# Kernel optimization log

Hardware: AMD Instinct MI355X
Metric: run time of the kernel (lower is better)

## Reference

```python
import jax, jax.numpy as jnp
import numpy as np

B, T, D = 64, 2048, 512
UNITS = 10  # hardcoded in original module


def setup_inputs() -> dict:
    key = jax.random.key(0)
    ks = jax.random.split(key, 6)
    Eo = jax.random.normal(ks[0], (B, T, D), dtype=jnp.float32)
    H = jax.random.normal(ks[1], (B, D), dtype=jnp.float32)
    # Keras Dense params: kernel [in, out], bias [out] (glorot-ish scale)
    W_eo = jax.random.normal(ks[2], (D, UNITS), dtype=jnp.float32) * (1.0 / np.sqrt(D))
    b_eo = jnp.zeros((UNITS,), dtype=jnp.float32)
    W_h = jax.random.normal(ks[3], (D, UNITS), dtype=jnp.float32) * (1.0 / np.sqrt(D))
    b_h = jnp.zeros((UNITS,), dtype=jnp.float32)
    W_s = jax.random.normal(ks[4], (UNITS, 1), dtype=jnp.float32) * (1.0 / np.sqrt(UNITS))
    b_s = jnp.zeros((1,), dtype=jnp.float32)
    return {"Eo": Eo, "H": H, "W_eo": W_eo, "b_eo": b_eo,
            "W_h": W_h, "b_h": b_h, "W_s": W_s, "b_s": b_s}


def reference(Eo, H, W_eo, b_eo, W_h, b_h, W_s, b_s):
    # Eo: [B, T, D], H: [B, D]
    Eo_d = jnp.einsum('btd,du->btu', Eo, W_eo) + b_eo          # [B, T, U]
    H_d = H @ W_h + b_h                                        # [B, U]
    EoH = jnp.tanh(Eo_d + H_d[:, None, :])                     # [B, T, U]
    score = jnp.einsum('btu,uo->bto', EoH, W_s) + b_s          # [B, T, 1]
    weight = jax.nn.softmax(score, axis=1)                     # softmax over T
    context = jnp.sum(Eo * weight, axis=1)                     # [B, D]
    return (context, weight)
```

## Files before the change

kernel.cpp:

```cpp
#include <hip/hip_runtime.h>
#include <math.h>

#define BB 64
#define TT 2048
#define DD 512
#define UU 10
#define S_CHUNKS 16
#define CHUNK_T (TT / S_CHUNKS)
#define NB (CHUNK_T / 16)

__device__ __forceinline__ float fast_tanh(float x) {
    return 1.0f - 2.0f / (1.0f + __expf(2.0f * x));
}

template<int K>
__device__ __forceinline__ float dpp_shr(float x) {
    int xi = __builtin_bit_cast(int, x);
    int r  = __builtin_amdgcn_update_dpp(0, xi, 0x110 | K, 0xF, 0xF, true);
    return __builtin_bit_cast(float, r);
}

__device__ __forceinline__ float read_lane_f(float v, int lane) {
    return __builtin_bit_cast(float,
        __builtin_amdgcn_readlane(__builtin_bit_cast(int, v), lane));
}

__global__ __launch_bounds__(256) void attn_pass1(
    const float* __restrict__ Eo, const float* __restrict__ H,
    const float* __restrict__ W_eo, const float* __restrict__ b_eo,
    const float* __restrict__ W_h, const float* __restrict__ b_h,
    const float* __restrict__ W_s, const float* __restrict__ b_s,
    float* __restrict__ pexp, float* __restrict__ pc)
{
    const int b     = blockIdx.y;
    const int chunk = blockIdx.x;
    const int tid   = threadIdx.x;
    const int wave  = tid >> 6;
    const int lane  = tid & 63;

    float hacc[UU];
    #pragma unroll
    for (int u = 0; u < UU; ++u) hacc[u] = 0.f;
    const float* Hb = H + (size_t)b * DD;
    #pragma unroll
    for (int k = 0; k < DD / 64; ++k) {
        float hv = Hb[k * 64 + lane];
        const float* wr = W_h + (size_t)(k * 64 + lane) * UU;
        #pragma unroll
        for (int u = 0; u < UU; ++u) hacc[u] += hv * wr[u];
    }
    #pragma unroll
    for (int off = 1; off < 64; off <<= 1) {
        #pragma unroll
        for (int u = 0; u < UU; ++u) hacc[u] += __shfl_xor(hacc[u], off, 64);
    }
    float hb[UU];
    #pragma unroll
    for (int u = 0; u < UU; ++u) hb[u] = hacc[u] + b_h[u] + b_eo[u];

    float wsv[UU];
    #pragma unroll
    for (int u = 0; u < UU; ++u) wsv[u] = W_s[u];
    const float bs = b_s[0];

    float wv[8][UU];
    #pragma unroll
    for (int k = 0; k < 2; ++k) {
        #pragma unroll
        for (int j = 0; j < 4; ++j) {
            const float* wr = W_eo + (size_t)(k * 256 + 4 * lane + j) * UU;
            #pragma unroll
            for (int u = 0; u < UU; ++u) wv[k * 4 + j][u] = wr[u];
        }
    }

    float l = 0.f;
    float c[8];
    #pragma unroll
    for (int j = 0; j < 8; ++j) c[j] = 0.f;

    const int  t0w  = chunk * CHUNK_T + wave * (CHUNK_T / 4);
    const bool lo32 = (lane & 32) == 0;
    const bool lo16 = (lane & 16) == 0;
    const float* rowbase = Eo + (size_t)b * TT * DD + 4 * lane;

    for (int i = 0; i < NB; ++i) {
        const int tb = t0w + i * 4;

        float e[4][8];
        #pragma unroll
        for (int tt = 0; tt < 4; ++tt) {
            const float* row = rowbase + (size_t)(tb + tt) * DD;
            float4 e0 = *(const float4*)(row);
            float4 e1 = *(const float4*)(row + 256);
            e[tt][0] = e0.x; e[tt][1] = e0.y; e[tt][2] = e0.z; e[tt][3] = e0.w;
            e[tt][4] = e1.x; e[tt][5] = e1.y; e[tt][6] = e1.z; e[tt][7] = e1.w;
        }

        float acc[4][UU];
        #pragma unroll
        for (int tt = 0; tt < 4; ++tt) {
            #pragma unroll
            for (int u = 0; u < UU; ++u) acc[tt][u] = 0.f;
            #pragma unroll
            for (int j = 0; j < 8; ++j) {
                #pragma unroll
                for (int u = 0; u < UU; ++u) acc[tt][u] += e[tt][j] * wv[j][u];
            }
        }

        float s = bs;
        #pragma unroll
        for (int u = 0; u < UU; ++u) {
            float y0 = lo32 ? acc[0][u] : acc[2][u];
            float o0 = lo32 ? acc[2][u] : acc[0][u];
            y0 += __shfl_xor(o0, 32, 64);
            float y1 = lo32 ? acc[1][u] : acc[3][u];
            float o1 = lo32 ? acc[3][u] : acc[1][u];
            y1 += __shfl_xor(o1, 32, 64);
            float z  = lo16 ? y0 : y1;
            float oz = lo16 ? y1 : y0;
            z += __shfl_xor(oz, 16, 64);
            z += dpp_shr<1>(z);
            z += dpp_shr<2>(z);
            z += dpp_shr<4>(z);
            z += dpp_shr<8>(z);
            s += wsv[u] * fast_tanh(z + hb[u]);
        }
        float p = __expf(s);

        if ((lane & 15) == 15) pexp[(size_t)b * TT + tb + (lane >> 4)] = p;

        float p0 = read_lane_f(p, 15);
        float p1 = read_lane_f(p, 31);
        float p2 = read_lane_f(p, 47);
        float p3 = read_lane_f(p, 63);
        l += (p0 + p1) + (p2 + p3);
        #pragma unroll
        for (int j = 0; j < 8; ++j)
            c[j] += p0 * e[0][j] + p1 * e[1][j] + p2 * e[2][j] + p3 * e[3][j];
    }

    __shared__ float sc[4][DD];
    #pragma unroll
    for (int k = 0; k < 2; ++k) {
        #pragma unroll
        for (int j = 0; j < 4; ++j)
            sc[wave][k * 256 + 4 * lane + j] = c[k * 4 + j];
    }
    __syncthreads();

    const int pidx = b * S_CHUNKS + chunk;
    for (int d = tid; d < DD; d += 256) {
        pc[(size_t)pidx * DD + d] = (sc[0][d] + sc[1][d]) + (sc[2][d] + sc[3][d]);
    }
}

__global__ __launch_bounds__(256) void attn_epilogue(
    const float* __restrict__ pexp, const float* __restrict__ pc,
    float* __restrict__ ctx_out, float* __restrict__ wout)
{
    const int b = blockIdx.x;
    const int tid = threadIdx.x;
    const int wave = tid >> 6;

    float s = 0.f;
    #pragma unroll
    for (int k = 0; k < TT / 256; ++k) s += pexp[(size_t)b * TT + k * 256 + tid];
    #pragma unroll
    for (int off = 1; off < 64; off <<= 1) s += __shfl_xor(s, off, 64);

    __shared__ float sl[4];
    if ((tid & 63) == 0) sl[wave] = s;
    __syncthreads();
    const float l = (sl[0] + sl[1]) + (sl[2] + sl[3]);
    const float inv = 1.0f / l;

    for (int d = tid; d < DD; d += 256) {
        float v = 0.f;
        #pragma unroll
        for (int sss = 0; sss < S_CHUNKS; ++sss)
            v += pc[((size_t)(b * S_CHUNKS + sss)) * DD + d];
        ctx_out[(size_t)b * DD + d] = v * inv;
    }
    for (int t = tid; t < TT; t += 256)
        wout[(size_t)b * TT + t] = pexp[(size_t)b * TT + t] * inv;
}

extern "C" void kernel_launch(void* const* d_in, const int* in_sizes, int n_in,
                              void* d_out, int out_size, void* d_ws, size_t ws_size,
                              hipStream_t stream) {
    const float* Eo   = (const float*)d_in[0];
    const float* H    = (const float*)d_in[1];
    const float* W_eo = (const float*)d_in[2];
    const float* b_eo = (const float*)d_in[3];
    const float* W_h  = (const float*)d_in[4];
    const float* b_h  = (const float*)d_in[5];
    const float* W_s  = (const float*)d_in[6];
    const float* b_s  = (const float*)d_in[7];

    float* pexp = (float*)d_ws;
    float* pc   = pexp + (size_t)BB * TT;

    float* out_ctx = (float*)d_out;
    float* out_w   = out_ctx + (size_t)BB * DD;

    dim3 gridA(S_CHUNKS, BB);
    attn_pass1<<<gridA, 256, 0, stream>>>(Eo, H, W_eo, b_eo, W_h, b_h, W_s, b_s,
                                          pexp, pc);
    attn_epilogue<<<BB, 256, 0, stream>>>(pexp, pc, out_ctx, out_w);
}
```

Measured before the change: 65.56 us.

## Process two timesteps per wave iteration and split epilogue across four blocks per batch

New measurement: 74.42 us. +13.5%, slower.

```diff
diff --git a/kernel.cpp b/kernel.cpp
--- a/kernel.cpp
+++ b/kernel.cpp
@@ -7,7 +7,7 @@
 #define UU 10
 #define S_CHUNKS 16
 #define CHUNK_T (TT / S_CHUNKS)
-#define NB (CHUNK_T / 16)
+#define NB (CHUNK_T / 8)
 
 __device__ __forceinline__ float fast_tanh(float x) {
     return 1.0f - 2.0f / (1.0f + __expf(2.0f * x));
@@ -81,15 +81,14 @@
 
     const int  t0w  = chunk * CHUNK_T + wave * (CHUNK_T / 4);
     const bool lo32 = (lane & 32) == 0;
-    const bool lo16 = (lane & 16) == 0;
     const float* rowbase = Eo + (size_t)b * TT * DD + 4 * lane;
 
     for (int i = 0; i < NB; ++i) {
-        const int tb = t0w + i * 4;
-
-        float e[4][8];
-        #pragma unroll
-        for (int tt = 0; tt < 4; ++tt) {
+        const int tb = t0w + i * 2;
+
+        float e[2][8];
+        #pragma unroll
+        for (int tt = 0; tt < 2; ++tt) {
             const float* row = rowbase + (size_t)(tb + tt) * DD;
             float4 e0 = *(const float4*)(row);
             float4 e1 = *(const float4*)(row + 256);
@@ -97,9 +96,9 @@
             e[tt][4] = e1.x; e[tt][5] = e1.y; e[tt][6] = e1.z; e[tt][7] = e1.w;
         }
 
-        float acc[4][UU];
-        #pragma unroll
-        for (int tt = 0; tt < 4; ++tt) {
+        float acc[2][UU];
+        #pragma unroll
+        for (int tt = 0; tt < 2; ++tt) {
             #pragma unroll
             for (int u = 0; u < UU; ++u) acc[tt][u] = 0.f;
             #pragma unroll
@@ -112,33 +111,27 @@
         float s = bs;
         #pragma unroll
         for (int u = 0; u < UU; ++u) {
-            float y0 = lo32 ? acc[0][u] : acc[2][u];
-            float o0 = lo32 ? acc[2][u] : acc[0][u];
-            y0 += __shfl_xor(o0, 32, 64);
-            float y1 = lo32 ? acc[1][u] : acc[3][u];
-            float o1 = lo32 ? acc[3][u] : acc[1][u];
-            y1 += __shfl_xor(o1, 32, 64);
-            float z  = lo16 ? y0 : y1;
-            float oz = lo16 ? y1 : y0;
-            z += __shfl_xor(oz, 16, 64);
-            z += dpp_shr<1>(z);
-            z += dpp_shr<2>(z);
-            z += dpp_shr<4>(z);
-            z += dpp_shr<8>(z);
-            s += wsv[u] * fast_tanh(z + hb[u]);
+            float y = lo32 ? acc[0][u] : acc[1][u];
+            float o = lo32 ? acc[1][u] : acc[0][u];
+            y += __shfl_xor(o, 32, 64);
+            y += __shfl_xor(y, 16, 64);
+            y += dpp_shr<1>(y);
+            y += dpp_shr<2>(y);
+            y += dpp_shr<4>(y);
+            y += dpp_shr<8>(y);
+            s += wsv[u] * fast_tanh(y + hb[u]);
         }
         float p = __expf(s);
 
-        if ((lane & 15) == 15) pexp[(size_t)b * TT + tb + (lane >> 4)] = p;
+        if (lane == 15) pexp[(size_t)b * TT + tb]     = p;
+        if (lane == 47) pexp[(size_t)b * TT + tb + 1] = p;
 
         float p0 = read_lane_f(p, 15);
-        float p1 = read_lane_f(p, 31);
-        float p2 = read_lane_f(p, 47);
-        float p3 = read_lane_f(p, 63);
-        l += (p0 + p1) + (p2 + p3);
+        float p1 = read_lane_f(p, 47);
+        l += p0 + p1;
         #pragma unroll
         for (int j = 0; j < 8; ++j)
-            c[j] += p0 * e[0][j] + p1 * e[1][j] + p2 * e[2][j] + p3 * e[3][j];
+            c[j] += p0 * e[0][j] + p1 * e[1][j];
     }
 
     __shared__ float sc[4][DD];
@@ -160,8 +153,9 @@
     const float* __restrict__ pexp, const float* __restrict__ pc,
     float* __restrict__ ctx_out, float* __restrict__ wout)
 {
-    const int b = blockIdx.x;
-    const int tid = threadIdx.x;
+    const int b    = blockIdx.x >> 2;
+    const int part = blockIdx.x & 3;
+    const int tid  = threadIdx.x;
     const int wave = tid >> 6;
 
     float s = 0.f;
@@ -176,15 +170,19 @@
     const float l = (sl[0] + sl[1]) + (sl[2] + sl[3]);
     const float inv = 1.0f / l;
 
-    for (int d = tid; d < DD; d += 256) {
+    const int d = part * (DD / 4) + tid;
+    if (tid < DD / 4) {
         float v = 0.f;
         #pragma unroll
         for (int sss = 0; sss < S_CHUNKS; ++sss)
             v += pc[((size_t)(b * S_CHUNKS + sss)) * DD + d];
         ctx_out[(size_t)b * DD + d] = v * inv;
     }
-    for (int t = tid; t < TT; t += 256)
+    #pragma unroll
+    for (int k = 0; k < 2; ++k) {
+        const int t = part * (TT / 4) + k * 256 + tid;
         wout[(size_t)b * TT + t] = pexp[(size_t)b * TT + t] * inv;
+    }
 }
 
 extern "C" void kernel_launch(void* const* d_in, const int* in_sizes, int n_in,
@@ -208,5 +206,5 @@
     dim3 gridA(S_CHUNKS, BB);
     attn_pass1<<<gridA, 256, 0, stream>>>(Eo, H, W_eo, b_eo, W_h, b_h, W_s, b_s,
                                           pexp, pc);
-    attn_epilogue<<<BB, 256, 0, stream>>>(pexp, pc, out_ctx, out_w);
-}
+    attn_epilogue<<<BB * 4, 256, 0, stream>>>(pexp, pc, out_ctx, out_w);
+}
```

## Double-buffer Eo rows via global_load_lds DMA and split epilogue across blocks

Applied to the files above, without the earlier changes.

Measured after the change: 65.32 us. About the same (-0.4%).

```diff
diff --git a/kernel.cpp b/kernel.cpp
--- a/kernel.cpp
+++ b/kernel.cpp
@@ -23,6 +23,12 @@
 __device__ __forceinline__ float read_lane_f(float v, int lane) {
     return __builtin_bit_cast(float,
         __builtin_amdgcn_readlane(__builtin_bit_cast(int, v), lane));
+}
+
+typedef __attribute__((address_space(1))) const void gvoid;
+typedef __attribute__((address_space(3))) void lvoid;
+__device__ __forceinline__ void dma16(const float* g, float* l) {
+    __builtin_amdgcn_global_load_lds((gvoid*)g, (lvoid*)l, 16, 0, 0);
 }
 
 __global__ __launch_bounds__(256) void attn_pass1(
@@ -38,6 +44,9 @@
     const int wave  = tid >> 6;
     const int lane  = tid & 63;
 
+    __shared__ __align__(16) float buf[4][2][4][DD];
+    __shared__ float sc[4][DD];
+
     float hacc[UU];
     #pragma unroll
     for (int u = 0; u < UU; ++u) hacc[u] = 0.f;
@@ -82,17 +91,33 @@
     const int  t0w  = chunk * CHUNK_T + wave * (CHUNK_T / 4);
     const bool lo32 = (lane & 32) == 0;
     const bool lo16 = (lane & 16) == 0;
-    const float* rowbase = Eo + (size_t)b * TT * DD + 4 * lane;
-
-    for (int i = 0; i < NB; ++i) {
+    const float* rowb = Eo + (size_t)b * TT * DD + 4 * lane;
+
+    #pragma unroll
+    for (int tt = 0; tt < 4; ++tt) {
+        const float* g = rowb + (size_t)(t0w + tt) * DD;
+        dma16(g,       &buf[wave][0][tt][0]);
+        dma16(g + 256, &buf[wave][0][tt][256]);
+    }
+
+    auto do_batch = [&](int i) {
+        const int cur = i & 1, nxt = cur ^ 1;
+        if (i + 1 < NB) {
+            #pragma unroll
+            for (int tt = 0; tt < 4; ++tt) {
+                const float* g = rowb + (size_t)(t0w + (i + 1) * 4 + tt) * DD;
+                dma16(g,       &buf[wave][nxt][tt][0]);
+                dma16(g + 256, &buf[wave][nxt][tt][256]);
+            }
+        }
+        __builtin_amdgcn_sched_barrier(0);
+
         const int tb = t0w + i * 4;
-
         float e[4][8];
         #pragma unroll
         for (int tt = 0; tt < 4; ++tt) {
-            const float* row = rowbase + (size_t)(tb + tt) * DD;
-            float4 e0 = *(const float4*)(row);
-            float4 e1 = *(const float4*)(row + 256);
+            float4 e0 = *(const float4*)&buf[wave][cur][tt][4 * lane];
+            float4 e1 = *(const float4*)&buf[wave][cur][tt][256 + 4 * lane];
             e[tt][0] = e0.x; e[tt][1] = e0.y; e[tt][2] = e0.z; e[tt][3] = e0.w;
             e[tt][4] = e1.x; e[tt][5] = e1.y; e[tt][6] = e1.z; e[tt][7] = e1.w;
         }
@@ -139,9 +164,17 @@
         #pragma unroll
         for (int j = 0; j < 8; ++j)
             c[j] += p0 * e[0][j] + p1 * e[1][j] + p2 * e[2][j] + p3 * e[3][j];
-    }
-
-    __shared__ float sc[4][DD];
+    };
+
+    asm volatile("s_waitcnt vmcnt(0)" ::: "memory");
+    __builtin_amdgcn_sched_barrier(0);
+    do_batch(0);
+    for (int i = 1; i < NB; ++i) {
+        asm volatile("s_waitcnt vmcnt(1)" ::: "memory");
+        __builtin_amdgcn_sched_barrier(0);
+        do_batch(i);
+    }
+
     #pragma unroll
     for (int k = 0; k < 2; ++k) {
         #pragma unroll
@@ -160,8 +193,9 @@
     const float* __restrict__ pexp, const float* __restrict__ pc,
     float* __restrict__ ctx_out, float* __restrict__ wout)
 {
-    const int b = blockIdx.x;
-    const int tid = threadIdx.x;
+    const int b    = blockIdx.x >> 2;
+    const int part = blockIdx.x & 3;
+    const int tid  = threadIdx.x;
     const int wave = tid >> 6;
 
     float s = 0.f;
@@ -176,15 +210,19 @@
     const float l = (sl[0] + sl[1]) + (sl[2] + sl[3]);
     const float inv = 1.0f / l;
 
-    for (int d = tid; d < DD; d += 256) {
+    const int d = part * (DD / 4) + tid;
+    if (tid < DD / 4) {
         float v = 0.f;
         #pragma unroll
         for (int sss = 0; sss < S_CHUNKS; ++sss)
             v += pc[((size_t)(b * S_CHUNKS + sss)) * DD + d];
         ctx_out[(size_t)b * DD + d] = v * inv;
     }
-    for (int t = tid; t < TT; t += 256)
+    #pragma unroll
+    for (int k = 0; k < 2; ++k) {
+        const int t = part * (TT / 4) + k * 256 + tid;
         wout[(size_t)b * TT + t] = pexp[(size_t)b * TT + t] * inv;
+    }
 }
 
 extern "C" void kernel_launch(void* const* d_in, const int* in_sizes, int n_in,
@@ -208,5 +246,5 @@
     dim3 gridA(S_CHUNKS, BB);
     attn_pass1<<<gridA, 256, 0, stream>>>(Eo, H, W_eo, b_eo, W_h, b_h, W_s, b_s,
                                           pexp, pc);
-    attn_epilogue<<<BB, 256, 0, stream>>>(pexp, pc, out_ctx, out_w);
-}
+    attn_epilogue<<<BB * 4, 256, 0, stream>>>(pexp, pc, out_ctx, out_w);
+}
```
